# Optimization experiments

Hardware: AMD Instinct MI355X
Metric: run time of the kernel (lower is better)

Reference implementation:

```python
import jax, jax.numpy as jnp
import numpy as np

N_NODES = 50000
D = 512
N_EDGES = 1600000

def setup_inputs() -> dict:
    key = jax.random.key(0)
    ks = jax.random.split(key, 5)
    x = jax.random.normal(ks[0], (N_NODES, D), dtype=jnp.float32)
    W = jax.random.normal(ks[1], (D, D), dtype=jnp.float32) * (1.0 / np.sqrt(D))
    b = jnp.zeros((D,), dtype=jnp.float32)
    edge_weight = jax.random.uniform(ks[2], (N_EDGES,), dtype=jnp.float32)
    edge_src = jax.random.randint(ks[3], (N_EDGES,), 0, N_NODES, dtype=jnp.int32)
    edge_dst = jax.random.randint(ks[4], (N_EDGES,), 0, N_NODES, dtype=jnp.int32)
    return {"x": x, "W": W, "b": b, "edge_weight": edge_weight,
            "edge_src": edge_src, "edge_dst": edge_dst}

def reference(x, W, b, edge_weight, edge_src, edge_dst):
    # GraphConvolution: support = x @ W; out = spmm(adj, support) + b
    support = x @ W                                  # [N, D] dense GEMM
    msgs = support[edge_src] * edge_weight[:, None]  # gather + scale [E, D]
    agg = jax.ops.segment_sum(msgs, edge_dst, num_segments=x.shape[0])  # [N, D]
    gc_out = agg + b
    # GCN2: relu then residual
    return jax.nn.relu(gc_out) + x
```

## Files before the change

### kernel.cpp

```cpp
#include <hip/hip_runtime.h>

#define N_NODES 50000
#define DIM 512
#define N_EDGES 1600000
#define CAP 96

typedef __attribute__((ext_vector_type(8))) short short8;
typedef __attribute__((ext_vector_type(8))) unsigned short ushort8;
typedef __attribute__((ext_vector_type(4))) float floatx4;

__device__ __forceinline__ unsigned short f2bf(float v) {
    unsigned u = __float_as_uint(v);
    unsigned r = u + 0x7FFF + ((u >> 16) & 1);
    return (unsigned short)(r >> 16);
}
__device__ __forceinline__ float bf2f(unsigned short h) {
    return __uint_as_float((unsigned)h << 16);
}
__device__ __forceinline__ void stage16(const char* g, char* l) {
    __builtin_amdgcn_global_load_lds((const __attribute__((address_space(1))) void*)g,
                                     (__attribute__((address_space(3))) void*)l, 16, 0, 0);
}

__global__ __launch_bounds__(256) void convert_x(const float* __restrict__ x,
                                                 unsigned short* __restrict__ xh,
                                                 unsigned short* __restrict__ xl) {
    const int t = blockIdx.x * 256 + threadIdx.x;
    if (t >= N_NODES * 64) return;
    const int row = t >> 6;
    const int kc = t & 63;
    const int blk = kc >> 3;
    const int c = kc & 7;
    const int cSw = c ^ (row & 7);

    const float4 v0 = *(const float4*)&x[row * DIM + kc * 8];
    const float4 v1 = *(const float4*)&x[row * DIM + kc * 8 + 4];
    float v[8] = {v0.x, v0.y, v0.z, v0.w, v1.x, v1.y, v1.z, v1.w};
    unsigned short h[8], l[8];
#pragma unroll
    for (int j = 0; j < 8; j++) {
        h[j] = f2bf(v[j]);
        l[j] = f2bf(v[j] - bf2f(h[j]));
    }
    const int o = row * DIM + blk * 64 + cSw * 8;
    *(short8*)&xh[o] = *(short8*)h;
    *(short8*)&xl[o] = *(short8*)l;
}

__global__ __launch_bounds__(256) void convert_w(const float* __restrict__ W,
                                                 unsigned short* __restrict__ wh,
                                                 unsigned short* __restrict__ wl) {
    const int t = blockIdx.x * 256 + threadIdx.x;
    if (t >= DIM * 64) return;
    const int n = t >> 6;
    const int kc = t & 63;
    const int blk = kc >> 3;
    const int c = kc & 7;
    const int cSw = c ^ (n & 7);

    unsigned short h[8], l[8];
#pragma unroll
    for (int j = 0; j < 8; j++) {
        const float v = W[(kc * 8 + j) * DIM + n];
        h[j] = f2bf(v);
        l[j] = f2bf(v - bf2f(h[j]));
    }
    const int o = n * DIM + blk * 64 + cSw * 8;
    *(short8*)&wh[o] = *(short8*)h;
    *(short8*)&wl[o] = *(short8*)l;
}

__global__ __launch_bounds__(256, 2) void gemm3(const unsigned short* __restrict__ xh,
                                                const unsigned short* __restrict__ xl,
                                                const unsigned short* __restrict__ wh,
                                                const unsigned short* __restrict__ wl,
                                                unsigned short* __restrict__ Cb, int M) {
    __shared__ __align__(128) char smem[65536];

    const int tid = threadIdx.x;
    const int row0 = blockIdx.y * 128;
    const int col0 = blockIdx.x * 128;

    int srow[4], schk[4];
#pragma unroll
    for (int i = 0; i < 4; i++) {
        const int q = i * 256 + tid;
        srow[i] = q >> 3;
        schk[i] = q & 7;
    }

    const int l = tid & 63;
    const int w = tid >> 6;
    const int wm = w & 1, wn = w >> 1;
    const int lrow = l & 15;
    const int kg = l >> 4;
    const int s = l & 7;

    int offA[4][2], offB[4][2];
#pragma unroll
    for (int mt = 0; mt < 4; mt++)
#pragma unroll
        for (int h = 0; h < 2; h++) {
            const int chunk = (kg + 4 * h) ^ s;
            offA[mt][h] = (wm * 64 + mt * 16 + lrow) * 128 + chunk * 16;
            offB[mt][h] = 32768 + (wn * 64 + mt * 16 + lrow) * 128 + chunk * 16;
        }

    floatx4 acc[4][4];
#pragma unroll
    for (int i = 0; i < 4; i++)
#pragma unroll
        for (int j = 0; j < 4; j++) acc[i][j] = (floatx4)(0.f);

    const char* xh8 = (const char*)xh;
    const char* xl8 = (const char*)xl;
    const char* wh8 = (const char*)wh;
    const char* wl8 = (const char*)wl;

    for (int kblk = 0; kblk < 8; kblk++) {
        __syncthreads();
#pragma unroll
        for (int i = 0; i < 4; i++) {
            const int q16 = (i * 256 + tid) * 16;
            const size_t ga = (size_t)min(row0 + srow[i], M - 1) * (DIM * 2)
                              + kblk * 128 + schk[i] * 16;
            const size_t gb = (size_t)(col0 + srow[i]) * (DIM * 2)
                              + kblk * 128 + schk[i] * 16;
            stage16(xh8 + ga, smem + q16);
            stage16(xl8 + ga, smem + 16384 + q16);
            stage16(wh8 + gb, smem + 32768 + q16);
            stage16(wl8 + gb, smem + 49152 + q16);
        }
        __syncthreads();

#pragma unroll
        for (int h = 0; h < 2; h++) {
            short8 bhf[4], blf[4];
#pragma unroll
            for (int nt = 0; nt < 4; nt++) {
                bhf[nt] = *(const short8*)(smem + offB[nt][h]);
                blf[nt] = *(const short8*)(smem + offB[nt][h] + 16384);
            }
#pragma unroll
            for (int mt = 0; mt < 4; mt++) {
                const short8 ahf = *(const short8*)(smem + offA[mt][h]);
                const short8 alf = *(const short8*)(smem + offA[mt][h] + 16384);
#pragma unroll
                for (int nt = 0; nt < 4; nt++) {
                    acc[mt][nt] = __builtin_amdgcn_mfma_f32_16x16x32_bf16(
                        ahf, bhf[nt], acc[mt][nt], 0, 0, 0);
                    acc[mt][nt] = __builtin_amdgcn_mfma_f32_16x16x32_bf16(
                        ahf, blf[nt], acc[mt][nt], 0, 0, 0);
                    acc[mt][nt] = __builtin_amdgcn_mfma_f32_16x16x32_bf16(
                        alf, bhf[nt], acc[mt][nt], 0, 0, 0);
                }
            }
        }
    }

    const int crow0 = row0 + wm * 64;
    const int ccol0 = col0 + wn * 64;
#pragma unroll
    for (int mt = 0; mt < 4; mt++) {
        const int rbase = crow0 + mt * 16 + kg * 4;
#pragma unroll
        for (int nt = 0; nt < 4; nt++) {
            const int cc = ccol0 + nt * 16 + lrow;
#pragma unroll
            for (int r = 0; r < 4; r++) {
                const int gr = rbase + r;
                if (gr < M) Cb[(size_t)gr * DIM + cc] = f2bf(acc[mt][nt][r]);
            }
        }
    }
}

__global__ __launch_bounds__(256) void gcn_build_edges(const int* __restrict__ esrc,
                                                       const int* __restrict__ edst,
                                                       const float* __restrict__ ew,
                                                       int* __restrict__ cursor,
                                                       uint2* __restrict__ table) {
    const int e = blockIdx.x * 256 + threadIdx.x;
    if (e >= N_EDGES) return;
    const int d = edst[e];
    const int pos = atomicAdd(&cursor[d], 1);
    if (pos < CAP) {
        table[d * CAP + pos] = make_uint2((unsigned)esrc[e], __float_as_uint(ew[e]));
    }
}

__global__ __launch_bounds__(64) void gcn_aggregate(const unsigned short* __restrict__ sup,
                                                    const int* __restrict__ cursor,
                                                    const uint2* __restrict__ table,
                                                    const float* __restrict__ x,
                                                    const float* __restrict__ b,
                                                    float* __restrict__ out) {
    const int n = blockIdx.x;
    const int tid = threadIdx.x;
    const int c = tid * 8;

    __shared__ uint2 s_e[CAP];
    const int deg = min(cursor[n], CAP);
    if (tid < deg) s_e[tid] = table[n * CAP + tid];
    if (tid + 64 < deg) s_e[tid + 64] = table[n * CAP + tid + 64];
    __syncthreads();

    float acc[8];
#pragma unroll
    for (int j = 0; j < 8; j++) acc[j] = 0.f;

#pragma unroll 4
    for (int i = 0; i < deg; i++) {
        const uint2 e = s_e[i];
        const float wt = __uint_as_float(e.y);
        const ushort8 v = *(const ushort8*)&sup[(size_t)e.x * DIM + c];
#pragma unroll
        for (int j = 0; j < 8; j++) acc[j] = fmaf(wt, bf2f(v[j]), acc[j]);
    }

    const floatx4 x0 = __builtin_nontemporal_load((const floatx4*)&x[n * DIM + c]);
    const floatx4 x1 = __builtin_nontemporal_load((const floatx4*)&x[n * DIM + c + 4]);
    const float4 b0 = *(const float4*)&b[c];
    const float4 b1 = *(const float4*)&b[c + 4];
    floatx4 o0, o1;
    o0.x = fmaxf(acc[0] + b0.x, 0.f) + x0.x;
    o0.y = fmaxf(acc[1] + b0.y, 0.f) + x0.y;
    o0.z = fmaxf(acc[2] + b0.z, 0.f) + x0.z;
    o0.w = fmaxf(acc[3] + b0.w, 0.f) + x0.w;
    o1.x = fmaxf(acc[4] + b1.x, 0.f) + x1.x;
    o1.y = fmaxf(acc[5] + b1.y, 0.f) + x1.y;
    o1.z = fmaxf(acc[6] + b1.z, 0.f) + x1.z;
    o1.w = fmaxf(acc[7] + b1.w, 0.f) + x1.w;
    __builtin_nontemporal_store(o0, (floatx4*)&out[n * DIM + c]);
    __builtin_nontemporal_store(o1, (floatx4*)&out[n * DIM + c + 4]);
}

extern "C" void kernel_launch(void* const* d_in, const int* in_sizes, int n_in,
                              void* d_out, int out_size, void* d_ws, size_t ws_size,
                              hipStream_t stream) {
    const float* x = (const float*)d_in[0];
    const float* W = (const float*)d_in[1];
    const float* b = (const float*)d_in[2];
    const float* ew = (const float*)d_in[3];
    const int* esrc = (const int*)d_in[4];
    const int* edst = (const int*)d_in[5];
    float* out = (float*)d_out;

    char* ws = (char*)d_ws;
    size_t off = 0;
    unsigned short* support = (unsigned short*)(ws + off); off += (size_t)N_NODES * DIM * 2;
    int* cursor = (int*)(ws + off);                   off += (size_t)N_NODES * 4;
    uint2* table = (uint2*)(ws + off);                off += (size_t)N_NODES * CAP * 8;
    unsigned short* xh = (unsigned short*)(ws + off); off += (size_t)N_NODES * DIM * 2;
    unsigned short* xl = (unsigned short*)(ws + off); off += (size_t)N_NODES * DIM * 2;
    unsigned short* wh = (unsigned short*)(ws + off); off += (size_t)DIM * DIM * 2;
    unsigned short* wl = (unsigned short*)(ws + off); off += (size_t)DIM * DIM * 2;

    (void)hipMemsetAsync(cursor, 0, (size_t)N_NODES * sizeof(int), stream);

    convert_w<<<(DIM * 64 + 255) / 256, 256, 0, stream>>>(W, wh, wl);
    convert_x<<<(N_NODES * 64 + 255) / 256, 256, 0, stream>>>(x, xh, xl);

    gcn_build_edges<<<(N_EDGES + 255) / 256, 256, 0, stream>>>(esrc, edst, ew,
                                                               cursor, table);

    dim3 gemm_grid(DIM / 128, (N_NODES + 127) / 128);
    gemm3<<<gemm_grid, 256, 0, stream>>>(xh, xl, wh, wl, support, N_NODES);

    gcn_aggregate<<<N_NODES, 64, 0, stream>>>(support, cursor, table, x, b, out);
}
```

Measured before the change: 659.8 us.

## Concatenate hi/lo bf16 along K, drop x_hi*W_lo term, read residual as bf16

The hi and lo bf16 parts of x are now packed into one K=1024 row, and W_hi is duplicated in a matching K=1024 layout. A single bf16 MFMA GEMM then computes x_hi*W_hi + x_lo*W_hi, which drops the x_hi*W_lo correction term and cuts matrix work to two thirds. Shared memory per block is halved, so the occupancy target rises to 3 blocks per CU. The aggregate kernel now reads the residual x from the bf16 hi copy instead of the fp32 input, halving those bytes. The cost is lower accuracy in both the GEMM and the residual add.

```diff
diff --git a/kernel.cpp b/kernel.cpp
--- a/kernel.cpp
+++ b/kernel.cpp
@@ -2,6 +2,7 @@
 
 #define N_NODES 50000
 #define DIM 512
+#define KCAT 1024
 #define N_EDGES 1600000
 #define CAP 96
 
@@ -23,8 +24,7 @@
 }
 
 __global__ __launch_bounds__(256) void convert_x(const float* __restrict__ x,
-                                                 unsigned short* __restrict__ xh,
-                                                 unsigned short* __restrict__ xl) {
+                                                 unsigned short* __restrict__ xcat) {
     const int t = blockIdx.x * 256 + threadIdx.x;
     if (t >= N_NODES * 64) return;
     const int row = t >> 6;
@@ -42,14 +42,13 @@
         h[j] = f2bf(v[j]);
         l[j] = f2bf(v[j] - bf2f(h[j]));
     }
-    const int o = row * DIM + blk * 64 + cSw * 8;
-    *(short8*)&xh[o] = *(short8*)h;
-    *(short8*)&xl[o] = *(short8*)l;
+    const int o = row * KCAT + blk * 64 + cSw * 8;
+    *(short8*)&xcat[o] = *(short8*)h;
+    *(short8*)&xcat[o + DIM] = *(short8*)l;
 }
 
 __global__ __launch_bounds__(256) void convert_w(const float* __restrict__ W,
-                                                 unsigned short* __restrict__ wh,
-                                                 unsigned short* __restrict__ wl) {
+                                                 unsigned short* __restrict__ wcat) {
     const int t = blockIdx.x * 256 + threadIdx.x;
     if (t >= DIM * 64) return;
     const int n = t >> 6;
@@ -58,24 +57,18 @@
     const int c = kc & 7;
     const int cSw = c ^ (n & 7);
 
-    unsigned short h[8], l[8];
-#pragma unroll
-    for (int j = 0; j < 8; j++) {
-        const float v = W[(kc * 8 + j) * DIM + n];
-        h[j] = f2bf(v);
-        l[j] = f2bf(v - bf2f(h[j]));
-    }
-    const int o = n * DIM + blk * 64 + cSw * 8;
-    *(short8*)&wh[o] = *(short8*)h;
-    *(short8*)&wl[o] = *(short8*)l;
-}
-
-__global__ __launch_bounds__(256, 2) void gemm3(const unsigned short* __restrict__ xh,
-                                                const unsigned short* __restrict__ xl,
-                                                const unsigned short* __restrict__ wh,
-                                                const unsigned short* __restrict__ wl,
-                                                unsigned short* __restrict__ Cb, int M) {
-    __shared__ __align__(128) char smem[65536];
+    unsigned short h[8];
+#pragma unroll
+    for (int j = 0; j < 8; j++) h[j] = f2bf(W[(kc * 8 + j) * DIM + n]);
+    const int o = n * KCAT + blk * 64 + cSw * 8;
+    *(short8*)&wcat[o] = *(short8*)h;
+    *(short8*)&wcat[o + DIM] = *(short8*)h;
+}
+
+__global__ __launch_bounds__(256, 3) void gemm_cat(const unsigned short* __restrict__ A,
+                                                   const unsigned short* __restrict__ B,
+                                                   unsigned short* __restrict__ Cb, int M) {
+    __shared__ __align__(128) char smem[32768];
 
     const int tid = threadIdx.x;
     const int row0 = blockIdx.y * 128;
@@ -103,7 +96,7 @@
         for (int h = 0; h < 2; h++) {
             const int chunk = (kg + 4 * h) ^ s;
             offA[mt][h] = (wm * 64 + mt * 16 + lrow) * 128 + chunk * 16;
-            offB[mt][h] = 32768 + (wn * 64 + mt * 16 + lrow) * 128 + chunk * 16;
+            offB[mt][h] = 16384 + (wn * 64 + mt * 16 + lrow) * 128 + chunk * 16;
         }
 
     floatx4 acc[4][4];
@@ -112,48 +105,35 @@
 #pragma unroll
         for (int j = 0; j < 4; j++) acc[i][j] = (floatx4)(0.f);
 
-    const char* xh8 = (const char*)xh;
-    const char* xl8 = (const char*)xl;
-    const char* wh8 = (const char*)wh;
-    const char* wl8 = (const char*)wl;
-
-    for (int kblk = 0; kblk < 8; kblk++) {
+    const char* A8 = (const char*)A;
+    const char* B8 = (const char*)B;
+
+    for (int kblk = 0; kblk < 16; kblk++) {
         __syncthreads();
 #pragma unroll
         for (int i = 0; i < 4; i++) {
             const int q16 = (i * 256 + tid) * 16;
-            const size_t ga = (size_t)min(row0 + srow[i], M - 1) * (DIM * 2)
+            const size_t ga = (size_t)min(row0 + srow[i], M - 1) * (KCAT * 2)
                               + kblk * 128 + schk[i] * 16;
-            const size_t gb = (size_t)(col0 + srow[i]) * (DIM * 2)
+            const size_t gb = (size_t)(col0 + srow[i]) * (KCAT * 2)
                               + kblk * 128 + schk[i] * 16;
-            stage16(xh8 + ga, smem + q16);
-            stage16(xl8 + ga, smem + 16384 + q16);
-            stage16(wh8 + gb, smem + 32768 + q16);
-            stage16(wl8 + gb, smem + 49152 + q16);
+            stage16(A8 + ga, smem + q16);
+            stage16(B8 + gb, smem + 16384 + q16);
         }
         __syncthreads();
 
 #pragma unroll
         for (int h = 0; h < 2; h++) {
-            short8 bhf[4], blf[4];
-#pragma unroll
-            for (int nt = 0; nt < 4; nt++) {
-                bhf[nt] = *(const short8*)(smem + offB[nt][h]);
-                blf[nt] = *(const short8*)(smem + offB[nt][h] + 16384);
-            }
+            short8 bf[4];
+#pragma unroll
+            for (int nt = 0; nt < 4; nt++) bf[nt] = *(const short8*)(smem + offB[nt][h]);
 #pragma unroll
             for (int mt = 0; mt < 4; mt++) {
-                const short8 ahf = *(const short8*)(smem + offA[mt][h]);
-                const short8 alf = *(const short8*)(smem + offA[mt][h] + 16384);
-#pragma unroll
-                for (int nt = 0; nt < 4; nt++) {
+                const short8 af = *(const short8*)(smem + offA[mt][h]);
+#pragma unroll
+                for (int nt = 0; nt < 4; nt++)
                     acc[mt][nt] = __builtin_amdgcn_mfma_f32_16x16x32_bf16(
-                        ahf, bhf[nt], acc[mt][nt], 0, 0, 0);
-                    acc[mt][nt] = __builtin_amdgcn_mfma_f32_16x16x32_bf16(
-                        ahf, blf[nt], acc[mt][nt], 0, 0, 0);
-                    acc[mt][nt] = __builtin_amdgcn_mfma_f32_16x16x32_bf16(
-                        alf, bhf[nt], acc[mt][nt], 0, 0, 0);
-                }
+                        af, bf[nt], acc[mt][nt], 0, 0, 0);
             }
         }
     }
@@ -192,7 +172,7 @@
 __global__ __launch_bounds__(64) void gcn_aggregate(const unsigned short* __restrict__ sup,
                                                     const int* __restrict__ cursor,
                                                     const uint2* __restrict__ table,
-                                                    const float* __restrict__ x,
+                                                    const unsigned short* __restrict__ xcat,
                                                     const float* __restrict__ b,
                                                     float* __restrict__ out) {
     const int n = blockIdx.x;
@@ -218,19 +198,17 @@
         for (int j = 0; j < 8; j++) acc[j] = fmaf(wt, bf2f(v[j]), acc[j]);
     }
 
-    const floatx4 x0 = __builtin_nontemporal_load((const floatx4*)&x[n * DIM + c]);
-    const floatx4 x1 = __builtin_nontemporal_load((const floatx4*)&x[n * DIM + c + 4]);
+    const int xoff = n * KCAT + (tid >> 3) * 64 + (((tid & 7) ^ (n & 7)) * 8);
+    const ushort8 xb = *(const ushort8*)&xcat[xoff];
     const float4 b0 = *(const float4*)&b[c];
     const float4 b1 = *(const float4*)&b[c + 4];
+    const float bb[8] = {b0.x, b0.y, b0.z, b0.w, b1.x, b1.y, b1.z, b1.w};
     floatx4 o0, o1;
-    o0.x = fmaxf(acc[0] + b0.x, 0.f) + x0.x;
-    o0.y = fmaxf(acc[1] + b0.y, 0.f) + x0.y;
-    o0.z = fmaxf(acc[2] + b0.z, 0.f) + x0.z;
-    o0.w = fmaxf(acc[3] + b0.w, 0.f) + x0.w;
-    o1.x = fmaxf(acc[4] + b1.x, 0.f) + x1.x;
-    o1.y = fmaxf(acc[5] + b1.y, 0.f) + x1.y;
-    o1.z = fmaxf(acc[6] + b1.z, 0.f) + x1.z;
-    o1.w = fmaxf(acc[7] + b1.w, 0.f) + x1.w;
+    float o[8];
+#pragma unroll
+    for (int j = 0; j < 8; j++) o[j] = fmaxf(acc[j] + bb[j], 0.f) + bf2f(xb[j]);
+    o0.x = o[0]; o0.y = o[1]; o0.z = o[2]; o0.w = o[3];
+    o1.x = o[4]; o1.y = o[5]; o1.z = o[6]; o1.w = o[7];
     __builtin_nontemporal_store(o0, (floatx4*)&out[n * DIM + c]);
     __builtin_nontemporal_store(o1, (floatx4*)&out[n * DIM + c + 4]);
 }
@@ -251,21 +229,19 @@
     unsigned short* support = (unsigned short*)(ws + off); off += (size_t)N_NODES * DIM * 2;
     int* cursor = (int*)(ws + off);                   off += (size_t)N_NODES * 4;
     uint2* table = (uint2*)(ws + off);                off += (size_t)N_NODES * CAP * 8;
-    unsigned short* xh = (unsigned short*)(ws + off); off += (size_t)N_NODES * DIM * 2;
-    unsigned short* xl = (unsigned short*)(ws + off); off += (size_t)N_NODES * DIM * 2;
-    unsigned short* wh = (unsigned short*)(ws + off); off += (size_t)DIM * DIM * 2;
-    unsigned short* wl = (unsigned short*)(ws + off); off += (size_t)DIM * DIM * 2;
+    unsigned short* xcat = (unsigned short*)(ws + off); off += (size_t)N_NODES * KCAT * 2;
+    unsigned short* wcat = (unsigned short*)(ws + off); off += (size_t)DIM * KCAT * 2;
 
     (void)hipMemsetAsync(cursor, 0, (size_t)N_NODES * sizeof(int), stream);
 
-    convert_w<<<(DIM * 64 + 255) / 256, 256, 0, stream>>>(W, wh, wl);
-    convert_x<<<(N_NODES * 64 + 255) / 256, 256, 0, stream>>>(x, xh, xl);
+    convert_w<<<(DIM * 64 + 255) / 256, 256, 0, stream>>>(W, wcat);
+    convert_x<<<(N_NODES * 64 + 255) / 256, 256, 0, stream>>>(x, xcat);
 
     gcn_build_edges<<<(N_EDGES + 255) / 256, 256, 0, stream>>>(esrc, edst, ew,
                                                                cursor, table);
 
     dim3 gemm_grid(DIM / 128, (N_NODES + 127) / 128);
-    gemm3<<<gemm_grid, 256, 0, stream>>>(xh, xl, wh, wl, support, N_NODES);
-
-    gcn_aggregate<<<N_NODES, 64, 0, stream>>>(support, cursor, table, x, b, out);
-}
+    gemm_cat<<<gemm_grid, 256, 0, stream>>>(xcat, wcat, support, N_NODES);
+
+    gcn_aggregate<<<N_NODES, 64, 0, stream>>>(support, cursor, table, xcat, b, out);
+}
```

Result: faster. 627.1 us (-5.0%).
